# Performance work log

Measured on AMD Instinct MI355X. Metric: run time of the kernel, lower is better.

The kernel has to match this reference:

```python
import jax, jax.numpy as jnp
import numpy as np

B, N, C, H = 2, 2048, 1024, 16
D = C // H  # head_dim = 64
EPS = 1e-6


def rmsnorm(x, w, eps=EPS):
    # RMSNorm over last dim (head_dim), matching torch RMSNorm (computed in fp32)
    x32 = x.astype(jnp.float32)
    y = x32 * jax.lax.rsqrt(jnp.mean(x32 * x32, axis=-1, keepdims=True) + eps)
    return y.astype(x.dtype) * w


def setup_inputs() -> dict:
    key = jax.random.key(0)
    ks = jax.random.split(key, 4)
    return {
        "x": jax.random.normal(ks[0], (B, N, C), dtype=jnp.float32),
        "w_qkv": jax.random.normal(ks[1], (C, 3 * C), dtype=jnp.float32) * 0.02,
        "b_qkv": jnp.zeros((3 * C,), dtype=jnp.float32),
        "q_w": jnp.ones((D,), dtype=jnp.float32),
        "k_w": jnp.ones((D,), dtype=jnp.float32),
        "w_proj": jax.random.normal(ks[2], (C, C), dtype=jnp.float32) * 0.02,
        "b_proj": jnp.zeros((C,), dtype=jnp.float32),
    }


def reference(x, w_qkv, b_qkv, q_w, k_w, w_proj, b_proj):
    b, n, c = x.shape
    h, d = H, c // H
    # QKV projection -> [3, B, H, N, D]
    qkv = (x @ w_qkv + b_qkv).reshape(b, n, 3, h, d).transpose(2, 0, 3, 1, 4)
    q, k, v = qkv[0], qkv[1], qkv[2]
    # per-head RMSNorm on q/k (qk_norm=True, use_rmsnorm=True)
    q = rmsnorm(q, q_w)
    k = rmsnorm(k, k_w)
    # scaled dot-product attention (scale = head_dim**-0.5, no dropout at eval)
    scale = d ** -0.5
    attn = jax.nn.softmax(jnp.einsum('bhqd,bhkd->bhqk', q, k) * scale, axis=-1)
    out = jnp.einsum('bhqk,bhkd->bhqd', attn, v)  # [B,H,N,D]
    out = out.transpose(0, 2, 1, 3).reshape(b, n, c)
    return out @ w_proj + b_proj
```

## Files before the change

kernel.cpp:

```cpp
#include <hip/hip_runtime.h>

typedef unsigned short u16;
typedef unsigned int u32;
typedef float f4 __attribute__((ext_vector_type(4)));
typedef __bf16 b8 __attribute__((ext_vector_type(8)));
typedef _Float16 h4 __attribute__((ext_vector_type(4)));
typedef __fp16 hp2 __attribute__((ext_vector_type(2)));

#if __has_builtin(__builtin_amdgcn_exp2f)
#define EXP2(x) __builtin_amdgcn_exp2f(x)
#else
#define EXP2(x) exp2f(x)
#endif

__device__ __forceinline__ u16 f2bf(float f) {
  unsigned u = __float_as_uint(f);
  u += 0x7fffu + ((u >> 16) & 1u);
  return (u16)(u >> 16);
}
__device__ __forceinline__ float bf2f(u16 h) {
  return __uint_as_float(((unsigned)h) << 16);
}

__global__ void k_convert_all(const float* __restrict__ x,
                              const float* __restrict__ w_qkv,
                              const float* __restrict__ w_proj,
                              u16* __restrict__ xb, u16* __restrict__ wqkT,
                              u16* __restrict__ wpjT) {
  __shared__ u16 t[64][65];
  int bid = blockIdx.x;
  if (bid < 2048) {
    int i = (bid * 256 + threadIdx.x) * 8;
    float4 a = *(const float4*)(x + i);
    float4 b = *(const float4*)(x + i + 4);
    union { u16 h[8]; uint4 v; } r;
    r.h[0] = f2bf(a.x); r.h[1] = f2bf(a.y); r.h[2] = f2bf(a.z); r.h[3] = f2bf(a.w);
    r.h[4] = f2bf(b.x); r.h[5] = f2bf(b.y); r.h[6] = f2bf(b.z); r.h[7] = f2bf(b.w);
    *(uint4*)(xb + i) = r.v;
    return;
  }
  const float* w; u16* wT; int Ncols, Krows, bx, by;
  if (bid < 2816) { int l = bid - 2048; w = w_qkv; wT = wqkT; Ncols = 3072; Krows = 1024; bx = l % 48; by = l / 48; }
  else            { int l = bid - 2816; w = w_proj; wT = wpjT; Ncols = 1024; Krows = 1024; bx = l & 15; by = l >> 4; }
  int n0 = bx * 64, k0 = by * 64;
#pragma unroll
  for (int it = 0; it < 16; ++it) {
    int e = it * 256 + threadIdx.x;
    int r = e >> 6, c = e & 63;
    t[r][c] = f2bf(w[(size_t)(k0 + r) * Ncols + n0 + c]);
  }
  __syncthreads();
#pragma unroll
  for (int it = 0; it < 4; ++it) {
    int e = it * 256 + threadIdx.x;
    int r = e >> 4, c0 = (e & 15) * 4;
    union { u16 h[4]; uint2 v; } pk;
    pk.h[0] = t[c0][r]; pk.h[1] = t[c0 + 1][r];
    pk.h[2] = t[c0 + 2][r]; pk.h[3] = t[c0 + 3][r];
    *(uint2*)(wT + (size_t)(n0 + r) * Krows + k0 + c0) = pk.v;
  }
}

__global__ __launch_bounds__(256, 3) void k_gemm_qkv(
    const u16* __restrict__ A, const u16* __restrict__ Bt,
    const float* __restrict__ bias,
    u16* __restrict__ oq, u16* __restrict__ ok, u16* __restrict__ ov,
    const float* __restrict__ qw, const float* __restrict__ kw,
    int K) {
  __shared__ u16 lA[2][128 * 32];
  __shared__ u16 lB[2][128 * 32];
  const int tid = threadIdx.x;
  const int lane = tid & 63, lrow = lane & 15, lq = lane >> 4;
  const int wave = tid >> 6;
  const int bm = blockIdx.y * 128, bn = blockIdx.x * 128;
  const int wm = (wave >> 1) * 64, wn = (wave & 1) * 64;

  const int ch0 = tid, ch1 = 256 + tid;
  const u16* ap0 = A + (size_t)(bm + (ch0 >> 2)) * K + (ch0 & 3) * 8;
  const u16* ap1 = A + (size_t)(bm + (ch1 >> 2)) * K + (ch1 & 3) * 8;
  const u16* bp0 = Bt + (size_t)(bn + (ch0 >> 2)) * K + (ch0 & 3) * 8;
  const u16* bp1 = Bt + (size_t)(bn + (ch1 >> 2)) * K + (ch1 & 3) * 8;

  uint4 pA0 = *(const uint4*)ap0, pA1 = *(const uint4*)ap1;
  uint4 pB0 = *(const uint4*)bp0, pB1 = *(const uint4*)bp1;

  f4 acc[4][4] = {};
  const int iters = K >> 5;
  for (int it = 0; it < iters; ++it) {
    const int s = it & 1;
    *(uint4*)(lA[s] + ch0 * 8) = pA0; *(uint4*)(lA[s] + ch1 * 8) = pA1;
    *(uint4*)(lB[s] + ch0 * 8) = pB0; *(uint4*)(lB[s] + ch1 * 8) = pB1;
    if (it + 1 < iters) {
      ap0 += 32; ap1 += 32; bp0 += 32; bp1 += 32;
      pA0 = *(const uint4*)ap0; pA1 = *(const uint4*)ap1;
      pB0 = *(const uint4*)bp0; pB1 = *(const uint4*)bp1;
    }
    __syncthreads();
    b8 af[4], bf[4];
#pragma unroll
    for (int i = 0; i < 4; ++i)
      af[i] = *(const b8*)(lA[s] + (wm + i * 16 + lrow) * 32 + lq * 8);
#pragma unroll
    for (int j = 0; j < 4; ++j)
      bf[j] = *(const b8*)(lB[s] + (wn + j * 16 + lrow) * 32 + lq * 8);
#pragma unroll
    for (int i = 0; i < 4; ++i)
#pragma unroll
      for (int j = 0; j < 4; ++j)
        acc[i][j] = __builtin_amdgcn_mfma_f32_16x16x32_bf16(af[i], bf[j], acc[i][j], 0, 0, 0);
  }

  float bv[4];
#pragma unroll
  for (int j = 0; j < 4; ++j) bv[j] = bias[bn + wn + j * 16 + lrow];

  const float CS = 0.125f * 1.44269504088896340736f;
  const int n0w = bn + wn;
  const int sec = n0w >> 10;
  const int h = (n0w >> 6) & 15;
#pragma unroll
  for (int i = 0; i < 4; ++i) {
    float v[4][4];
#pragma unroll
    for (int j = 0; j < 4; ++j)
#pragma unroll
      for (int r = 0; r < 4; ++r) v[j][r] = acc[i][j][r] + bv[j];
    if (sec < 2) {
      u16* dst = sec == 0 ? oq : ok;
      const float* w = sec == 0 ? qw : kw;
      float ex = sec == 0 ? CS : 1.0f;
#pragma unroll
      for (int r = 0; r < 4; ++r) {
        float ss = v[0][r] * v[0][r] + v[1][r] * v[1][r] +
                   v[2][r] * v[2][r] + v[3][r] * v[3][r];
        ss += __shfl_xor(ss, 1, 64); ss += __shfl_xor(ss, 2, 64);
        ss += __shfl_xor(ss, 4, 64); ss += __shfl_xor(ss, 8, 64);
        float sc = rsqrtf(ss * (1.0f / 64.0f) + 1e-6f) * ex;
        int m = bm + wm + i * 16 + lq * 4 + r;
        int bb = m >> 11, ns = m & 2047;
        u16* rowp = dst + ((size_t)(bb * 16 + h) * 2048 + ns) * 64;
#pragma unroll
        for (int j = 0; j < 4; ++j) {
          int d = j * 16 + lrow;
          rowp[d] = f2bf(v[j][r] * sc * w[d]);
        }
      }
    } else {
      int m0 = bm + wm + i * 16 + lq * 4;
      int bb = m0 >> 11, ns = m0 & 2047;
#pragma unroll
      for (int j = 0; j < 4; ++j) {
        int d = j * 16 + lrow;
        union { _Float16 hh[4]; uint2 u; } pk;
#pragma unroll
        for (int r = 0; r < 4; ++r) pk.hh[r] = (_Float16)v[j][r];
        *(uint2*)(ov + ((size_t)(bb * 16 + h) * 64 + d) * 2048 + ns) = pk.u;
      }
    }
  }
}

__global__ __launch_bounds__(256, 4) void k_gemm2(
    const u16* __restrict__ A, const u16* __restrict__ Bt,
    const float* __restrict__ bias, float* __restrict__ outF,
    int K, int Ncols) {
  __shared__ u16 lA[2][64 * 32];
  __shared__ u16 lB[2][128 * 32];
  const int tid = threadIdx.x;
  const int lane = tid & 63, lrow = lane & 15, lq = lane >> 4;
  const int wave = tid >> 6;
  const int bm = blockIdx.y * 64, bn = blockIdx.x * 128;
  const int wm = (wave >> 1) * 32, wn = (wave & 1) * 64;

  const int cha = tid;
  const int ch0 = tid, ch1 = 256 + tid;
  const u16* ap = A + (size_t)(bm + (cha >> 2)) * K + (cha & 3) * 8;
  const u16* bp0 = Bt + (size_t)(bn + (ch0 >> 2)) * K + (ch0 & 3) * 8;
  const u16* bp1 = Bt + (size_t)(bn + (ch1 >> 2)) * K + (ch1 & 3) * 8;

  uint4 pA = *(const uint4*)ap;
  uint4 pB0 = *(const uint4*)bp0, pB1 = *(const uint4*)bp1;

  f4 acc[2][4] = {};
  const int iters = K >> 5;
  for (int it = 0; it < iters; ++it) {
    const int s = it & 1;
    *(uint4*)(lA[s] + cha * 8) = pA;
    *(uint4*)(lB[s] + ch0 * 8) = pB0; *(uint4*)(lB[s] + ch1 * 8) = pB1;
    if (it + 1 < iters) {
      ap += 32; bp0 += 32; bp1 += 32;
      pA = *(const uint4*)ap;
      pB0 = *(const uint4*)bp0; pB1 = *(const uint4*)bp1;
    }
    __syncthreads();
    b8 af[2], bf[4];
#pragma unroll
    for (int i = 0; i < 2; ++i)
      af[i] = *(const b8*)(lA[s] + (wm + i * 16 + lrow) * 32 + lq * 8);
#pragma unroll
    for (int j = 0; j < 4; ++j)
      bf[j] = *(const b8*)(lB[s] + (wn + j * 16 + lrow) * 32 + lq * 8);
#pragma unroll
    for (int i = 0; i < 2; ++i)
#pragma unroll
      for (int j = 0; j < 4; ++j)
        acc[i][j] = __builtin_amdgcn_mfma_f32_16x16x32_bf16(af[i], bf[j], acc[i][j], 0, 0, 0);
  }
#pragma unroll
  for (int i = 0; i < 2; ++i)
#pragma unroll
    for (int j = 0; j < 4; ++j) {
      int n = bn + wn + j * 16 + lrow;
      float bv = bias[n];
#pragma unroll
      for (int r = 0; r < 4; ++r) {
        int m = bm + wm + i * 16 + lq * 4 + r;
        outF[(size_t)m * Ncols + n] = acc[i][j][r] + bv;
      }
    }
}

__global__ __launch_bounds__(512, 2) void k_attn(
    const u16* __restrict__ qb, const u16* __restrict__ kb,
    const u16* __restrict__ vt, u16* __restrict__ ao) {
  __shared__ u16 lK[128 * 72];
  __shared__ u16 lV[64 * 140];
  const int bh = blockIdx.y;
  const int q0 = blockIdx.x * 256;
  const int tid = threadIdx.x, wave = tid >> 6, lane = tid & 63;
  const int lrow = lane & 15, lq = lane >> 4;
  const int wq = wave * 32;

  b8 qf[2][2];
#pragma unroll
  for (int g = 0; g < 2; ++g)
#pragma unroll
    for (int ks = 0; ks < 2; ++ks)
      qf[g][ks] = *(const b8*)(qb + ((size_t)bh * 2048 + q0 + wq + g * 16 + lrow) * 64 +
                               ks * 32 + lq * 8);

  f4 o[2][4] = {};
  f4 lacc[2] = {};
  h4 ones;
  ones[0] = (_Float16)1.0f; ones[1] = (_Float16)1.0f;
  ones[2] = (_Float16)1.0f; ones[3] = (_Float16)1.0f;

  const int ch0 = tid, ch1 = 512 + tid;
  const u16* kp0 = kb + (size_t)bh * 2048 * 64 + (size_t)(ch0 >> 3) * 64 + (ch0 & 7) * 8;
  const u16* kp1 = kb + (size_t)bh * 2048 * 64 + (size_t)(ch1 >> 3) * 64 + (ch1 & 7) * 8;
  const u16* vp0 = vt + (size_t)bh * 64 * 2048 + (size_t)(ch0 >> 4) * 2048 + (ch0 & 15) * 8;
  const u16* vp1 = vt + (size_t)bh * 64 * 2048 + (size_t)(ch1 >> 4) * 2048 + (ch1 & 15) * 8;
  u16* lKw0 = lK + (ch0 >> 3) * 72 + (ch0 & 7) * 8;
  u16* lKw1 = lK + (ch1 >> 3) * 72 + (ch1 & 7) * 8;
  u16* lVw0 = lV + (ch0 >> 4) * 140 + (ch0 & 15) * 8;
  u16* lVw1 = lV + (ch1 >> 4) * 140 + (ch1 & 15) * 8;

  uint4 pK0 = *(const uint4*)kp0, pK1 = *(const uint4*)kp1;
  uint4 pV0 = *(const uint4*)vp0, pV1 = *(const uint4*)vp1;

  for (int it = 0; it < 16; ++it) {
    *(uint4*)lKw0 = pK0;
    *(uint4*)lKw1 = pK1;
    *(uint2*)lVw0 = make_uint2(pV0.x, pV0.y);
    *(uint2*)(lVw0 + 4) = make_uint2(pV0.z, pV0.w);
    *(uint2*)lVw1 = make_uint2(pV1.x, pV1.y);
    *(uint2*)(lVw1 + 4) = make_uint2(pV1.z, pV1.w);
    __syncthreads();

    if (it < 15) {
      kp0 += 128 * 64; kp1 += 128 * 64; vp0 += 128; vp1 += 128;
      pK0 = *(const uint4*)kp0; pK1 = *(const uint4*)kp1;
      pV0 = *(const uint4*)vp0; pV1 = *(const uint4*)vp1;
    }

    f4 st[2][8] = {};
#pragma unroll
    for (int ks = 0; ks < 2; ++ks)
#pragma unroll
      for (int kt = 0; kt < 8; ++kt) {
        b8 kf = *(const b8*)(lK + (kt * 16 + lrow) * 72 + ks * 32 + lq * 8);
        st[0][kt] = __builtin_amdgcn_mfma_f32_16x16x32_bf16(kf, qf[0][ks], st[0][kt], 0, 0, 0);
        st[1][kt] = __builtin_amdgcn_mfma_f32_16x16x32_bf16(kf, qf[1][ks], st[1][kt], 0, 0, 0);
      }

    h4 pf[2][8];
#pragma unroll
    for (int g = 0; g < 2; ++g)
#pragma unroll
      for (int kt = 0; kt < 8; ++kt) {
        union { hp2 p2[2]; h4 v; } cv;
        cv.p2[0] = __builtin_amdgcn_cvt_pkrtz(EXP2(st[g][kt][0]), EXP2(st[g][kt][1]));
        cv.p2[1] = __builtin_amdgcn_cvt_pkrtz(EXP2(st[g][kt][2]), EXP2(st[g][kt][3]));
        pf[g][kt] = cv.v;
      }

#pragma unroll
    for (int kt = 0; kt < 8; ++kt) {
      lacc[0] = __builtin_amdgcn_mfma_f32_16x16x16f16(ones, pf[0][kt], lacc[0], 0, 0, 0);
      lacc[1] = __builtin_amdgcn_mfma_f32_16x16x16f16(ones, pf[1][kt], lacc[1], 0, 0, 0);
#pragma unroll
      for (int dt = 0; dt < 4; ++dt) {
        h4 va = *(const h4*)(lV + (dt * 16 + lrow) * 140 + kt * 16 + lq * 4);
        o[0][dt] = __builtin_amdgcn_mfma_f32_16x16x16f16(va, pf[0][kt], o[0][dt], 0, 0, 0);
        o[1][dt] = __builtin_amdgcn_mfma_f32_16x16x16f16(va, pf[1][kt], o[1][dt], 0, 0, 0);
      }
    }
    __syncthreads();
  }

  const int bb = bh >> 4, h = bh & 15;
#pragma unroll
  for (int g = 0; g < 2; ++g) {
    float inv = 1.0f / lacc[g][0];
    int q = q0 + wq + g * 16 + lrow;
#pragma unroll
    for (int dt = 0; dt < 4; ++dt) {
      union { u16 h2[4]; uint2 v; } r;
#pragma unroll
      for (int rr = 0; rr < 4; ++rr) r.h2[rr] = f2bf(o[g][dt][rr] * inv);
      *(uint2*)(ao + ((size_t)bb * 2048 + q) * 1024 + h * 64 + dt * 16 + lq * 4) = r.v;
    }
  }
}

extern "C" void kernel_launch(void* const* d_in, const int* in_sizes, int n_in,
                              void* d_out, int out_size, void* d_ws, size_t ws_size,
                              hipStream_t stream) {
  const float* x      = (const float*)d_in[0];
  const float* w_qkv  = (const float*)d_in[1];
  const float* b_qkv  = (const float*)d_in[2];
  const float* q_w    = (const float*)d_in[3];
  const float* k_w    = (const float*)d_in[4];
  const float* w_proj = (const float*)d_in[5];
  const float* b_proj = (const float*)d_in[6];
  float* out = (float*)d_out;

  u16* xb   = (u16*)d_ws;
  u16* wqkT = xb + 4194304;
  u16* wpjT = wqkT + 3145728;
  u16* qb   = wpjT + 1048576;
  u16* kb   = qb + 4194304;
  u16* vtb  = kb + 4194304;
  u16* ao   = xb;

  k_convert_all<<<3072, 256, 0, stream>>>(x, w_qkv, w_proj, xb, wqkT, wpjT);
  k_gemm_qkv<<<dim3(24, 32), 256, 0, stream>>>(xb, wqkT, b_qkv, qb, kb, vtb, q_w, k_w, 1024);
  k_attn<<<dim3(8, 32), 512, 0, stream>>>(qb, kb, vtb, ao);
  k_gemm2<<<dim3(8, 64), 256, 0, stream>>>(ao, wpjT, b_proj, out, 1024, 1024);
}
```

Measured before the change: 189.7 us.

## Drop LDS staging in attention; load K/V fragments directly from global

The attention kernel no longer stages K and V tiles through shared memory with barriers. Each wave now loads its MFMA K and V fragments straight from global memory (relying on L2/L1 for reuse across waves) in 64-key steps. The block shrinks to 256 threads covering 128 queries, so the grid doubles. This removes LDS writes and __syncthreads, but every wave now issues redundant global loads with less coalescing and no software prefetch.

```diff
diff --git a/kernel.cpp b/kernel.cpp
--- a/kernel.cpp
+++ b/kernel.cpp
@@ -220,13 +220,11 @@
     }
 }
 
-__global__ __launch_bounds__(512, 2) void k_attn(
+__global__ __launch_bounds__(256, 2) void k_attn(
     const u16* __restrict__ qb, const u16* __restrict__ kb,
     const u16* __restrict__ vt, u16* __restrict__ ao) {
-  __shared__ u16 lK[128 * 72];
-  __shared__ u16 lV[64 * 140];
   const int bh = blockIdx.y;
-  const int q0 = blockIdx.x * 256;
+  const int q0 = blockIdx.x * 128;
   const int tid = threadIdx.x, wave = tid >> 6, lane = tid & 63;
   const int lrow = lane & 15, lq = lane >> 4;
   const int wq = wave * 32;
@@ -245,49 +243,31 @@
   ones[0] = (_Float16)1.0f; ones[1] = (_Float16)1.0f;
   ones[2] = (_Float16)1.0f; ones[3] = (_Float16)1.0f;
 
-  const int ch0 = tid, ch1 = 512 + tid;
-  const u16* kp0 = kb + (size_t)bh * 2048 * 64 + (size_t)(ch0 >> 3) * 64 + (ch0 & 7) * 8;
-  const u16* kp1 = kb + (size_t)bh * 2048 * 64 + (size_t)(ch1 >> 3) * 64 + (ch1 & 7) * 8;
-  const u16* vp0 = vt + (size_t)bh * 64 * 2048 + (size_t)(ch0 >> 4) * 2048 + (ch0 & 15) * 8;
-  const u16* vp1 = vt + (size_t)bh * 64 * 2048 + (size_t)(ch1 >> 4) * 2048 + (ch1 & 15) * 8;
-  u16* lKw0 = lK + (ch0 >> 3) * 72 + (ch0 & 7) * 8;
-  u16* lKw1 = lK + (ch1 >> 3) * 72 + (ch1 & 7) * 8;
-  u16* lVw0 = lV + (ch0 >> 4) * 140 + (ch0 & 15) * 8;
-  u16* lVw1 = lV + (ch1 >> 4) * 140 + (ch1 & 15) * 8;
-
-  uint4 pK0 = *(const uint4*)kp0, pK1 = *(const uint4*)kp1;
-  uint4 pV0 = *(const uint4*)vp0, pV1 = *(const uint4*)vp1;
-
-  for (int it = 0; it < 16; ++it) {
-    *(uint4*)lKw0 = pK0;
-    *(uint4*)lKw1 = pK1;
-    *(uint2*)lVw0 = make_uint2(pV0.x, pV0.y);
-    *(uint2*)(lVw0 + 4) = make_uint2(pV0.z, pV0.w);
-    *(uint2*)lVw1 = make_uint2(pV1.x, pV1.y);
-    *(uint2*)(lVw1 + 4) = make_uint2(pV1.z, pV1.w);
-    __syncthreads();
-
-    if (it < 15) {
-      kp0 += 128 * 64; kp1 += 128 * 64; vp0 += 128; vp1 += 128;
-      pK0 = *(const uint4*)kp0; pK1 = *(const uint4*)kp1;
-      pV0 = *(const uint4*)vp0; pV1 = *(const uint4*)vp1;
-    }
-
-    f4 st[2][8] = {};
+  const u16* krow = kb + (size_t)bh * 2048 * 64 + (size_t)lrow * 64 + lq * 8;
+  const u16* vrow = vt + (size_t)bh * 64 * 2048 + (size_t)lrow * 2048 + lq * 4;
+
+  for (int kt0 = 0; kt0 < 2048; kt0 += 64) {
+    b8 kfa[2][4];
 #pragma unroll
     for (int ks = 0; ks < 2; ++ks)
 #pragma unroll
-      for (int kt = 0; kt < 8; ++kt) {
-        b8 kf = *(const b8*)(lK + (kt * 16 + lrow) * 72 + ks * 32 + lq * 8);
-        st[0][kt] = __builtin_amdgcn_mfma_f32_16x16x32_bf16(kf, qf[0][ks], st[0][kt], 0, 0, 0);
-        st[1][kt] = __builtin_amdgcn_mfma_f32_16x16x32_bf16(kf, qf[1][ks], st[1][kt], 0, 0, 0);
-      }
-
-    h4 pf[2][8];
+      for (int kt = 0; kt < 4; ++kt)
+        kfa[ks][kt] = *(const b8*)(krow + (size_t)(kt0 + kt * 16) * 64 + ks * 32);
+
+    f4 st[2][4] = {};
+#pragma unroll
+    for (int ks = 0; ks < 2; ++ks)
+#pragma unroll
+      for (int kt = 0; kt < 4; ++kt) {
+        st[0][kt] = __builtin_amdgcn_mfma_f32_16x16x32_bf16(kfa[ks][kt], qf[0][ks], st[0][kt], 0, 0, 0);
+        st[1][kt] = __builtin_amdgcn_mfma_f32_16x16x32_bf16(kfa[ks][kt], qf[1][ks], st[1][kt], 0, 0, 0);
+      }
+
+    h4 pf[2][4];
 #pragma unroll
     for (int g = 0; g < 2; ++g)
 #pragma unroll
-      for (int kt = 0; kt < 8; ++kt) {
+      for (int kt = 0; kt < 4; ++kt) {
         union { hp2 p2[2]; h4 v; } cv;
         cv.p2[0] = __builtin_amdgcn_cvt_pkrtz(EXP2(st[g][kt][0]), EXP2(st[g][kt][1]));
         cv.p2[1] = __builtin_amdgcn_cvt_pkrtz(EXP2(st[g][kt][2]), EXP2(st[g][kt][3]));
@@ -295,17 +275,16 @@
       }
 
 #pragma unroll
-    for (int kt = 0; kt < 8; ++kt) {
+    for (int kt = 0; kt < 4; ++kt) {
       lacc[0] = __builtin_amdgcn_mfma_f32_16x16x16f16(ones, pf[0][kt], lacc[0], 0, 0, 0);
       lacc[1] = __builtin_amdgcn_mfma_f32_16x16x16f16(ones, pf[1][kt], lacc[1], 0, 0, 0);
 #pragma unroll
       for (int dt = 0; dt < 4; ++dt) {
-        h4 va = *(const h4*)(lV + (dt * 16 + lrow) * 140 + kt * 16 + lq * 4);
+        h4 va = *(const h4*)(vrow + (size_t)dt * 16 * 2048 + kt0 + kt * 16);
         o[0][dt] = __builtin_amdgcn_mfma_f32_16x16x16f16(va, pf[0][kt], o[0][dt], 0, 0, 0);
         o[1][dt] = __builtin_amdgcn_mfma_f32_16x16x16f16(va, pf[1][kt], o[1][dt], 0, 0, 0);
       }
     }
-    __syncthreads();
   }
 
   const int bb = bh >> 4, h = bh & 15;
@@ -345,6 +324,6 @@
 
   k_convert_all<<<3072, 256, 0, stream>>>(x, w_qkv, w_proj, xb, wqkT, wpjT);
   k_gemm_qkv<<<dim3(24, 32), 256, 0, stream>>>(xb, wqkT, b_qkv, qb, kb, vtb, q_w, k_w, 1024);
-  k_attn<<<dim3(8, 32), 512, 0, stream>>>(qb, kb, vtb, ao);
+  k_attn<<<dim3(16, 32), 256, 0, stream>>>(qb, kb, vtb, ao);
   k_gemm2<<<dim3(8, 64), 256, 0, stream>>>(ao, wpjT, b_proj, out, 1024, 1024);
 }
```

After: 310.3 us. 63.6% more time.
